# Kernel tuning notes

Hardware: AMD Instinct MI355X
Metric: run time of the kernel (lower is better)

## Reference

```python
import jax, jax.numpy as jnp
import numpy as np

B, S, H, DH = 2, 4096, 8, 64
D = H * DH


def setup_inputs() -> dict:
    key = jax.random.key(0)
    ks = jax.random.split(key, 6)
    std = 1.0 / np.sqrt(D)
    return {
        "x": jax.random.normal(ks[0], (B, S, D), dtype=jnp.float32),
        "Wq": jax.random.normal(ks[1], (D, D), dtype=jnp.float32) * std,
        "Wk": jax.random.normal(ks[2], (D, D), dtype=jnp.float32) * std,
        "Wv": jax.random.normal(ks[3], (D, D), dtype=jnp.float32) * std,
        "Wo": jax.random.normal(ks[4], (D, D), dtype=jnp.float32) * std,
        "bo": jnp.zeros((D,), dtype=jnp.float32),
    }


def reference(x, Wq, Wk, Wv, Wo, bo):
    scale = DH ** (-0.5)
    # torch Linear: y = x @ W.T
    q = x @ Wq.T  # [B,S,D]
    k = x @ Wk.T
    v = x @ Wv.T
    # split heads -> [B,H,S,Dh]
    q = q.reshape(B, S, H, DH).transpose(0, 2, 1, 3)
    k = k.reshape(B, S, H, DH).transpose(0, 2, 1, 3)
    v = v.reshape(B, S, H, DH).transpose(0, 2, 1, 3)
    score = jnp.einsum('bhqd,bhkd->bhqk', q, k) * scale  # [B,H,S,S]
    weights = jax.nn.softmax(score, axis=-1)
    attn = jnp.einsum('bhqk,bhkd->bhqd', weights, v)  # [B,H,S,Dh]
    h_ = attn.transpose(0, 2, 1, 3).reshape(B, S, D)
    return h_ @ Wo.T + bo
```

## Files before the change

### kernel.cpp

```cpp
#include <hip/hip_runtime.h>

#define LOG2E 1.44269504088896340736f

typedef unsigned short u16;
typedef __bf16 bf16x4_t __attribute__((ext_vector_type(4)));
typedef __bf16 bf16x8_t __attribute__((ext_vector_type(8)));
typedef float f32x4_t __attribute__((ext_vector_type(4)));

__device__ __forceinline__ f32x4_t mfma16(bf16x8_t a, bf16x8_t b, f32x4_t c) {
  return __builtin_amdgcn_mfma_f32_16x16x32_bf16(a, b, c, 0, 0, 0);
}

__device__ __forceinline__ void gl_lds16(const u16* g, u16* l) {
  __builtin_amdgcn_global_load_lds(
      (const __attribute__((address_space(1))) unsigned int*)g,
      (__attribute__((address_space(3))) unsigned int*)l, 16, 0, 0);
}

__global__ __launch_bounds__(256) void cast_kernel(
    const float* __restrict__ x, const float* __restrict__ Wq, const float* __restrict__ Wk,
    const float* __restrict__ Wv, const float* __restrict__ Wo,
    u16* __restrict__ Xb, u16* __restrict__ Wqb, u16* __restrict__ Wkb,
    u16* __restrict__ Wvb, u16* __restrict__ Wob) {
  const int bid = blockIdx.x;
  const float* src;
  u16* dst;
  float scale = 1.f;
  int rel;
  if (bid < 2048)      { src = x;  dst = Xb;  rel = bid; }
  else if (bid < 2176) { src = Wq; dst = Wqb; rel = bid - 2048; scale = 0.125f * LOG2E; }
  else if (bid < 2304) { src = Wk; dst = Wkb; rel = bid - 2176; }
  else if (bid < 2432) { src = Wv; dst = Wvb; rel = bid - 2304; }
  else                 { src = Wo; dst = Wob; rel = bid - 2432; }
  const int i = rel * 2048 + threadIdx.x * 8;
  f32x4_t a = *(const f32x4_t*)(src + i) * scale;
  f32x4_t b = *(const f32x4_t*)(src + i + 4) * scale;
  union { uint4 u; struct { bf16x4_t lo, hi; } s; } c;
  c.s.lo = __builtin_convertvector(a, bf16x4_t);
  c.s.hi = __builtin_convertvector(b, bf16x4_t);
  *(uint4*)(dst + i) = c.u;
}

template <int MODE>
__device__ __forceinline__ void gemm_core_bf16(const u16* __restrict__ A, const u16* __restrict__ Bt,
                                               void* __restrict__ Cout, const float* __restrict__ bo,
                                               int Mbase, int Nbase) {
  __shared__ __align__(16) u16 smem[128 * 128];
  u16 (*As)[64] = (u16(*)[64])smem;
  u16 (*Bs)[64] = (u16(*)[64])(smem + 128 * 64);
  const int t = threadIdx.x;
  const int wave = t >> 6, lane = t & 63;
  const int r = lane & 15, qd = lane >> 4;
  const int wm = wave & 1, wn = wave >> 1;
  const int rr = lane >> 3;
  const int s8 = ((lane & 7) ^ (rr & 7)) * 8;

  f32x4_t acc[4][4];
#pragma unroll
  for (int i = 0; i < 4; i++)
#pragma unroll
    for (int j = 0; j < 4; j++) { f32x4_t z = {0.f, 0.f, 0.f, 0.f}; acc[i][j] = z; }

  const u16* pa = A  + (Mbase + wave * 32 + rr) * 512 + s8;
  const u16* pb = Bt + (Nbase + wave * 32 + rr) * 512 + s8;
  u16* la = &As[wave * 32][0];
  u16* lb = &Bs[wave * 32][0];

  for (int k0 = 0; k0 < 512; k0 += 64) {
#pragma unroll
    for (int j = 0; j < 4; j++) gl_lds16(pa + k0 + j * 8 * 512, la + j * 8 * 64);
#pragma unroll
    for (int j = 0; j < 4; j++) gl_lds16(pb + k0 + j * 8 * 512, lb + j * 8 * 64);
    __syncthreads();
#pragma unroll
    for (int h = 0; h < 2; h++) {
      bf16x8_t af[4], bfr[4];
#pragma unroll
      for (int i = 0; i < 4; i++)
        af[i]  = *(const bf16x8_t*)&As[wm * 64 + i * 16 + r][((h * 4 + qd) ^ (r & 7)) * 8];
#pragma unroll
      for (int j = 0; j < 4; j++)
        bfr[j] = *(const bf16x8_t*)&Bs[wn * 64 + j * 16 + r][((h * 4 + qd) ^ (r & 7)) * 8];
#pragma unroll
      for (int i = 0; i < 4; i++)
#pragma unroll
        for (int j = 0; j < 4; j++) acc[i][j] = mfma16(af[i], bfr[j], acc[i][j]);
    }
    __syncthreads();
  }

  if (MODE != 2) {
#pragma unroll
    for (int i = 0; i < 4; i++)
#pragma unroll
      for (int j = 0; j < 4; j++)
#pragma unroll
        for (int reg = 0; reg < 4; reg++) {
          int row = wm * 64 + i * 16 + qd * 4 + reg;
          int col = wn * 64 + j * 16 + r;
          __bf16 bv = (__bf16)acc[i][j][reg];
          smem[row * 128 + (col ^ (((row >> 2) & 7) << 3))] = *(u16*)&bv;
        }
    __syncthreads();
#pragma unroll
    for (int p = 0; p < 8; p++) {
      int row = p * 16 + (t >> 4);
      int col = (t & 15) * 8;
      uint4 v = *(const uint4*)&smem[row * 128 + (col ^ (((row >> 2) & 7) << 3))];
      if (MODE == 0) {
        *(uint4*)&((u16*)Cout)[(Mbase + row) * 512 + Nbase + col] = v;
      } else {
        int bb = Nbase >> 12;
        int ss = (Nbase & 4095) + col;
        *(uint4*)&((u16*)Cout)[((long)(bb * 512 + Mbase + row)) * 4096 + ss] = v;
      }
    }
  } else {
    float* stf = (float*)smem;
    float bv[4];
#pragma unroll
    for (int j = 0; j < 4; j++) bv[j] = bo[Nbase + wn * 64 + j * 16 + r];
#pragma unroll
    for (int hh = 0; hh < 2; hh++) {
      __syncthreads();
      if (wm == hh) {
#pragma unroll
        for (int i = 0; i < 4; i++)
#pragma unroll
          for (int j = 0; j < 4; j++)
#pragma unroll
            for (int reg = 0; reg < 4; reg++) {
              int row = i * 16 + qd * 4 + reg;
              int col = wn * 64 + j * 16 + r;
              stf[row * 128 + (col ^ (((row >> 2) & 7) << 2))] = acc[i][j][reg] + bv[j];
            }
      }
      __syncthreads();
#pragma unroll
      for (int p = 0; p < 4; p++) {
        int row = p * 16 + (t >> 4);
        int col = (t & 15) * 8;
        f32x4_t v0 = *(const f32x4_t*)&stf[row * 128 + ((col) ^ (((row >> 2) & 7) << 2))];
        f32x4_t v1 = *(const f32x4_t*)&stf[row * 128 + ((col + 4) ^ (((row >> 2) & 7) << 2))];
        *(f32x4_t*)&((float*)Cout)[(Mbase + hh * 64 + row) * 512 + Nbase + col] = v0;
        *(f32x4_t*)&((float*)Cout)[(Mbase + hh * 64 + row) * 512 + Nbase + col + 4] = v1;
      }
    }
  }
}

__global__ __launch_bounds__(256) void gemm_qkv_kernel(
    const u16* __restrict__ Xb,
    const u16* __restrict__ Wqb, const u16* __restrict__ Wkb, const u16* __restrict__ Wvb,
    u16* __restrict__ Q, u16* __restrict__ K, u16* __restrict__ Vt) {
  if (blockIdx.z == 0)
    gemm_core_bf16<0>(Xb, Wqb, Q, nullptr, blockIdx.x * 128, blockIdx.y * 128);
  else if (blockIdx.z == 1)
    gemm_core_bf16<0>(Xb, Wkb, K, nullptr, blockIdx.x * 128, blockIdx.y * 128);
  else
    gemm_core_bf16<1>(Wvb, Xb, Vt, nullptr, blockIdx.y * 128, blockIdx.x * 128);
}

__global__ __launch_bounds__(256) void gemm_out_kernel(
    const u16* __restrict__ Aat, const u16* __restrict__ Wob,
    float* __restrict__ Out, const float* __restrict__ bo) {
  gemm_core_bf16<2>(Aat, Wob, Out, bo, blockIdx.x * 128, blockIdx.y * 128);
}

__global__ __launch_bounds__(512, 2) void attn_kernel(
    const u16* __restrict__ Q, const u16* __restrict__ K, const u16* __restrict__ Vt,
    u16* __restrict__ Oattn) {
  __shared__ __align__(16) u16 KVs[32768];
  __shared__ float Lsc2[1024];
#define KS(kvv, bf) (KVs + ((kvv) * 2 + (bf)) * 4096)
#define VS(kvv, bf) (KVs + 16384 + ((kvv) * 2 + (bf)) * 4096)

  const int t = threadIdx.x;
  const int wave = t >> 6, lane = t & 63;
  const int r = lane & 15, qd = lane >> 4;
  const int g = wave >> 1, kv = wave & 1;

  const int flat = blockIdx.y * 16 + blockIdx.x;
  const int xcd = flat & 7, idx = flat >> 3;
  const int bh = xcd * 2 + (idx >> 4);
  const int qi = idx & 15;
  const int b = bh >> 3, h = bh & 7;
  const long bbase = (long)b * 4096 * 512;
  const int q0 = qi * 256;

  const int sw = r & 7;
  const int ck0 = (qd ^ sw) * 8;
  const int ck1 = ((qd + 4) ^ sw) * 8;
  int vo0[2], vo1[2];
#pragma unroll
  for (int c = 0; c < 2; c++) {
    vo0[c] = ((c * 4 + (qd >> 1)) ^ sw) * 8 + 4 * (qd & 1);
    vo1[c] = ((c * 4 + 2 + (qd >> 1)) ^ sw) * 8 + 4 * (qd & 1);
  }

  bf16x8_t ones8;
#pragma unroll
  for (int j = 0; j < 8; j++) ones8[j] = (__bf16)1.0f;

  bf16x8_t qf[4][2];
#pragma unroll
  for (int qa = 0; qa < 4; qa++) {
    const u16* qp = Q + bbase + (long)(q0 + g * 64 + qa * 16 + r) * 512 + h * 64 + qd * 8;
    qf[qa][0] = *(const bf16x8_t*)(qp);
    qf[qa][1] = *(const bf16x8_t*)(qp + 32);
  }

  f32x4_t accO[4][4];
  f32x4_t accL[4];
#pragma unroll
  for (int qa = 0; qa < 4; qa++) {
    f32x4_t z = {0.f, 0.f, 0.f, 0.f};
    accL[qa] = z;
#pragma unroll
    for (int nt = 0; nt < 4; nt++) accO[qa][nt] = z;
  }

  const int rr = lane >> 3;
  const int cc = (lane & 7) ^ rr;
  const u16* kgb = K + bbase + (long)(kv * 2048 + g * 16 + rr) * 512 + h * 64 + cc * 8;
  const u16* vgb = Vt + ((long)(b * 512 + h * 64 + g * 16 + rr)) * 4096 + kv * 2048 + cc * 8;

#pragma unroll
  for (int i = 0; i < 2; i++) gl_lds16(kgb + (long)i * 8 * 512, KS(kv, 0) + g * 1024 + i * 512);
#pragma unroll
  for (int i = 0; i < 2; i++) gl_lds16(vgb + (long)i * 8 * 4096, VS(kv, 0) + g * 1024 + i * 512);

  for (int it = 0; it < 32; it++) {
    const int buf = it & 1;
    __syncthreads();

    if (it < 31) {
      const int nb = (it + 1) & 1;
      const long ko = (long)(it + 1) * 64;
#pragma unroll
      for (int i = 0; i < 2; i++)
        gl_lds16(kgb + (ko + i * 8) * 512, KS(kv, nb) + g * 1024 + i * 512);
#pragma unroll
      for (int i = 0; i < 2; i++)
        gl_lds16(vgb + ko + (long)i * 8 * 4096, VS(kv, nb) + g * 1024 + i * 512);
    }

    bf16x8_t kf[4][2];
#pragma unroll
    for (int nt = 0; nt < 4; nt++) {
      const u16* kb = KS(kv, buf) + (nt * 16 + r) * 64;
      kf[nt][0] = *(const bf16x8_t*)(kb + ck0);
      kf[nt][1] = *(const bf16x8_t*)(kb + ck1);
    }

    f32x4_t St[4][4];
    __builtin_amdgcn_s_setprio(1);
#pragma unroll
    for (int qa = 0; qa < 4; qa++)
#pragma unroll
      for (int nt = 0; nt < 4; nt++) {
        f32x4_t z = {0.f, 0.f, 0.f, 0.f};
        z = mfma16(kf[nt][0], qf[qa][0], z);
        z = mfma16(kf[nt][1], qf[qa][1], z);
        St[qa][nt] = z;
      }
    __builtin_amdgcn_s_setprio(0);

    bf16x8_t pf[4][2];
#pragma unroll
    for (int qa = 0; qa < 4; qa++)
#pragma unroll
      for (int c = 0; c < 2; c++) {
        f32x4_t e0, e1;
#pragma unroll
        for (int j = 0; j < 4; j++) {
          e0[j] = __builtin_amdgcn_exp2f(St[qa][2 * c][j]);
          e1[j] = __builtin_amdgcn_exp2f(St[qa][2 * c + 1][j]);
        }
        bf16x4_t b0 = __builtin_convertvector(e0, bf16x4_t);
        bf16x4_t b1 = __builtin_convertvector(e1, bf16x4_t);
        bf16x8_t p8;
#pragma unroll
        for (int j = 0; j < 4; j++) { p8[j] = b0[j]; p8[4 + j] = b1[j]; }
        pf[qa][c] = p8;
      }

#pragma unroll
    for (int qa = 0; qa < 4; qa++)
#pragma unroll
      for (int c = 0; c < 2; c++)
        accL[qa] = mfma16(ones8, pf[qa][c], accL[qa]);

#pragma unroll
    for (int c = 0; c < 2; c++) {
      bf16x8_t va[4];
#pragma unroll
      for (int dm = 0; dm < 4; dm++) {
        const u16* vb = VS(kv, buf) + (dm * 16 + r) * 64;
        union { uint4 u; bf16x8_t v; } cat;
        *(uint2*)&cat.u.x = *(const uint2*)(vb + vo0[c]);
        *(uint2*)&cat.u.z = *(const uint2*)(vb + vo1[c]);
        va[dm] = cat.v;
      }
      __builtin_amdgcn_s_setprio(1);
#pragma unroll
      for (int qa = 0; qa < 4; qa++)
#pragma unroll
        for (int dm = 0; dm < 4; dm++)
          accO[qa][dm] = mfma16(va[dm], pf[qa][c], accO[qa][dm]);
      __builtin_amdgcn_s_setprio(0);
    }
  }

  __syncthreads();
  float* Sc = (float*)KVs;
  if (kv == 1) {
#pragma unroll
    for (int qa = 0; qa < 4; qa++) {
#pragma unroll
      for (int dm = 0; dm < 4; dm++)
        *(f32x4_t*)&Sc[g * 4096 + ((qa * 4 + dm) * 64 + lane) * 4] = accO[qa][dm];
      Lsc2[g * 256 + qa * 64 + lane] = accL[qa][0];
    }
  }
  __syncthreads();
  if (kv == 0) {
#pragma unroll
    for (int qa = 0; qa < 4; qa++) {
      float L = accL[qa][0] + Lsc2[g * 256 + qa * 64 + lane];
      float inv = 1.f / L;
      int gq = q0 + g * 64 + qa * 16 + r;
#pragma unroll
      for (int dm = 0; dm < 4; dm++) {
        f32x4_t o = *(const f32x4_t*)&Sc[g * 4096 + ((qa * 4 + dm) * 64 + lane) * 4];
        o += accO[qa][dm];
        bf16x4_t ob;
#pragma unroll
        for (int reg = 0; reg < 4; reg++) ob[reg] = (__bf16)(o[reg] * inv);
        *(uint2*)&Oattn[bbase + (long)gq * 512 + h * 64 + dm * 16 + qd * 4] = *(uint2*)&ob;
      }
    }
  }
#undef KS
#undef VS
}

extern "C" void kernel_launch(void* const* d_in, const int* in_sizes, int n_in,
                              void* d_out, int out_size, void* d_ws, size_t ws_size,
                              hipStream_t stream) {
  const float* x  = (const float*)d_in[0];
  const float* Wq = (const float*)d_in[1];
  const float* Wk = (const float*)d_in[2];
  const float* Wv = (const float*)d_in[3];
  const float* Wo = (const float*)d_in[4];
  const float* bo = (const float*)d_in[5];
  float* out = (float*)d_out;

  u16* ws  = (u16*)d_ws;
  u16* Qb  = ws;
  u16* Kb  = Qb  + 4194304;
  u16* Vtg = Kb  + 4194304;
  u16* Ab  = Vtg + 4194304;
  u16* Xb  = Ab;
  u16* Wqb = Ab  + 4194304;
  u16* Wkb = Wqb + 262144;
  u16* Wvb = Wkb + 262144;
  u16* Wob = Wvb + 262144;

  cast_kernel<<<2560, 256, 0, stream>>>(x, Wq, Wk, Wv, Wo, Xb, Wqb, Wkb, Wvb, Wob);

  dim3 g1(64, 4, 3);
  gemm_qkv_kernel<<<g1, 256, 0, stream>>>(Xb, Wqb, Wkb, Wvb, Qb, Kb, Vtg);

  dim3 g2(16, 16);
  attn_kernel<<<g2, 512, 0, stream>>>(Qb, Kb, Vtg, Ab);

  dim3 g3(64, 4);
  gemm_out_kernel<<<g3, 256, 0, stream>>>(Ab, Wob, out, bo);
}
```

Before: 192.3 us.

## Software-pipeline QK^T one tile ahead with triple-buffered K in attention

Restructures the attention loop so the QK^T scores for the next KV tile are computed while the softmax exp and PV MFMAs of the current tile run. K is triple-buffered in LDS (prefetched two tiles ahead) and V stays double-buffered, which raises LDS use per block. The aim is to overlap exp/VALU work with matrix-core work and hide LDS latency. It costs extra registers for two score sets, which risks spills or lower occupancy under launch_bounds(512,2).

```diff
diff --git a/kernel.cpp b/kernel.cpp
--- a/kernel.cpp
+++ b/kernel.cpp
@@ -170,10 +170,8 @@
 __global__ __launch_bounds__(512, 2) void attn_kernel(
     const u16* __restrict__ Q, const u16* __restrict__ K, const u16* __restrict__ Vt,
     u16* __restrict__ Oattn) {
-  __shared__ __align__(16) u16 KVs[32768];
+  __shared__ __align__(16) u16 KVs[40960];
   __shared__ float Lsc2[1024];
-#define KS(kvv, bf) (KVs + ((kvv) * 2 + (bf)) * 4096)
-#define VS(kvv, bf) (KVs + 16384 + ((kvv) * 2 + (bf)) * 4096)
 
   const int t = threadIdx.x;
   const int wave = t >> 6, lane = t & 63;
@@ -191,11 +189,11 @@
   const int sw = r & 7;
   const int ck0 = (qd ^ sw) * 8;
   const int ck1 = ((qd + 4) ^ sw) * 8;
-  int vo0[2], vo1[2];
+  int vof0[2], vof1[2];
 #pragma unroll
   for (int c = 0; c < 2; c++) {
-    vo0[c] = ((c * 4 + (qd >> 1)) ^ sw) * 8 + 4 * (qd & 1);
-    vo1[c] = ((c * 4 + 2 + (qd >> 1)) ^ sw) * 8 + 4 * (qd & 1);
+    vof0[c] = ((c * 4 + (qd >> 1)) ^ sw) * 8 + 4 * (qd & 1);
+    vof1[c] = ((c * 4 + 2 + (qd >> 1)) ^ sw) * 8 + 4 * (qd & 1);
   }
 
   bf16x8_t ones8;
@@ -224,82 +222,98 @@
   const int cc = (lane & 7) ^ rr;
   const u16* kgb = K + bbase + (long)(kv * 2048 + g * 16 + rr) * 512 + h * 64 + cc * 8;
   const u16* vgb = Vt + ((long)(b * 512 + h * 64 + g * 16 + rr)) * 4096 + kv * 2048 + cc * 8;
-
-#pragma unroll
-  for (int i = 0; i < 2; i++) gl_lds16(kgb + (long)i * 8 * 512, KS(kv, 0) + g * 1024 + i * 512);
-#pragma unroll
-  for (int i = 0; i < 2; i++) gl_lds16(vgb + (long)i * 8 * 4096, VS(kv, 0) + g * 1024 + i * 512);
-
-  for (int it = 0; it < 32; it++) {
-    const int buf = it & 1;
-    __syncthreads();
-
+  u16* kst = KVs + kv * 4096 + g * 1024;
+  u16* vst = KVs + 24576 + kv * 4096 + g * 1024;
+  const u16* krd = KVs + kv * 4096;
+  const u16* vrd = KVs + 24576 + kv * 4096;
+
+#pragma unroll
+  for (int i = 0; i < 2; i++) gl_lds16(kgb + (long)i * 8 * 512, kst + i * 512);
+#pragma unroll
+  for (int i = 0; i < 2; i++) gl_lds16(kgb + (long)(64 + i * 8) * 512, kst + 8192 + i * 512);
+#pragma unroll
+  for (int i = 0; i < 2; i++) gl_lds16(vgb + (long)i * 8 * 4096, vst + i * 512);
+  __syncthreads();
+
+  f32x4_t Sa[4][4], Sb[4][4];
+
+  __builtin_amdgcn_s_setprio(1);
+#pragma unroll
+  for (int nt = 0; nt < 4; nt++) {
+    const u16* kb = krd + (nt * 16 + r) * 64;
+    bf16x8_t kf0 = *(const bf16x8_t*)(kb + ck0);
+    bf16x8_t kf1 = *(const bf16x8_t*)(kb + ck1);
+#pragma unroll
+    for (int qa = 0; qa < 4; qa++) {
+      f32x4_t z = {0.f, 0.f, 0.f, 0.f};
+      z = mfma16(kf0, qf[qa][0], z);
+      z = mfma16(kf1, qf[qa][1], z);
+      Sa[qa][nt] = z;
+    }
+  }
+  __builtin_amdgcn_s_setprio(0);
+
+  int kr = 1, kw = 2;
+
+  auto body = [&](int it, f32x4_t (&Sp)[4][4], f32x4_t (&Sn)[4][4]) {
+    if (it < 30) {
+      const long ko = (long)(it + 2) * 64;
+      u16* kd = kst + kw * 8192;
+#pragma unroll
+      for (int i = 0; i < 2; i++) gl_lds16(kgb + (ko + i * 8) * 512, kd + i * 512);
+    }
     if (it < 31) {
-      const int nb = (it + 1) & 1;
-      const long ko = (long)(it + 1) * 64;
-#pragma unroll
-      for (int i = 0; i < 2; i++)
-        gl_lds16(kgb + (ko + i * 8) * 512, KS(kv, nb) + g * 1024 + i * 512);
-#pragma unroll
-      for (int i = 0; i < 2; i++)
-        gl_lds16(vgb + ko + (long)i * 8 * 4096, VS(kv, nb) + g * 1024 + i * 512);
-    }
-
-    bf16x8_t kf[4][2];
-#pragma unroll
-    for (int nt = 0; nt < 4; nt++) {
-      const u16* kb = KS(kv, buf) + (nt * 16 + r) * 64;
-      kf[nt][0] = *(const bf16x8_t*)(kb + ck0);
-      kf[nt][1] = *(const bf16x8_t*)(kb + ck1);
-    }
-
-    f32x4_t St[4][4];
-    __builtin_amdgcn_s_setprio(1);
-#pragma unroll
-    for (int qa = 0; qa < 4; qa++)
+      const long vo = (long)(it + 1) * 64;
+      u16* vd = vst + ((it + 1) & 1) * 8192;
+#pragma unroll
+      for (int i = 0; i < 2; i++) gl_lds16(vgb + vo + (long)i * 8 * 4096, vd + i * 512);
+    }
+    if (it < 31) {
+      const u16* kbb = krd + kr * 8192;
+      __builtin_amdgcn_s_setprio(1);
 #pragma unroll
       for (int nt = 0; nt < 4; nt++) {
-        f32x4_t z = {0.f, 0.f, 0.f, 0.f};
-        z = mfma16(kf[nt][0], qf[qa][0], z);
-        z = mfma16(kf[nt][1], qf[qa][1], z);
-        St[qa][nt] = z;
-      }
-    __builtin_amdgcn_s_setprio(0);
-
-    bf16x8_t pf[4][2];
-#pragma unroll
-    for (int qa = 0; qa < 4; qa++)
-#pragma unroll
-      for (int c = 0; c < 2; c++) {
+        const u16* kb = kbb + (nt * 16 + r) * 64;
+        bf16x8_t kf0 = *(const bf16x8_t*)(kb + ck0);
+        bf16x8_t kf1 = *(const bf16x8_t*)(kb + ck1);
+#pragma unroll
+        for (int qa = 0; qa < 4; qa++) {
+          f32x4_t z = {0.f, 0.f, 0.f, 0.f};
+          z = mfma16(kf0, qf[qa][0], z);
+          z = mfma16(kf1, qf[qa][1], z);
+          Sn[qa][nt] = z;
+        }
+      }
+      __builtin_amdgcn_s_setprio(0);
+    }
+    const u16* vbb = vrd + (it & 1) * 8192;
+#pragma unroll
+    for (int c = 0; c < 2; c++) {
+      bf16x8_t pf[4];
+#pragma unroll
+      for (int qa = 0; qa < 4; qa++) {
         f32x4_t e0, e1;
 #pragma unroll
         for (int j = 0; j < 4; j++) {
-          e0[j] = __builtin_amdgcn_exp2f(St[qa][2 * c][j]);
-          e1[j] = __builtin_amdgcn_exp2f(St[qa][2 * c + 1][j]);
+          e0[j] = __builtin_amdgcn_exp2f(Sp[qa][2 * c][j]);
+          e1[j] = __builtin_amdgcn_exp2f(Sp[qa][2 * c + 1][j]);
         }
         bf16x4_t b0 = __builtin_convertvector(e0, bf16x4_t);
         bf16x4_t b1 = __builtin_convertvector(e1, bf16x4_t);
         bf16x8_t p8;
 #pragma unroll
         for (int j = 0; j < 4; j++) { p8[j] = b0[j]; p8[4 + j] = b1[j]; }
-        pf[qa][c] = p8;
-      }
-
-#pragma unroll
-    for (int qa = 0; qa < 4; qa++)
-#pragma unroll
-      for (int c = 0; c < 2; c++)
-        accL[qa] = mfma16(ones8, pf[qa][c], accL[qa]);
-
-#pragma unroll
-    for (int c = 0; c < 2; c++) {
+        pf[qa] = p8;
+      }
+#pragma unroll
+      for (int qa = 0; qa < 4; qa++) accL[qa] = mfma16(ones8, pf[qa], accL[qa]);
       bf16x8_t va[4];
 #pragma unroll
       for (int dm = 0; dm < 4; dm++) {
-        const u16* vb = VS(kv, buf) + (dm * 16 + r) * 64;
+        const u16* vb = vbb + (dm * 16 + r) * 64;
         union { uint4 u; bf16x8_t v; } cat;
-        *(uint2*)&cat.u.x = *(const uint2*)(vb + vo0[c]);
-        *(uint2*)&cat.u.z = *(const uint2*)(vb + vo1[c]);
+        *(uint2*)&cat.u.x = *(const uint2*)(vb + vof0[c]);
+        *(uint2*)&cat.u.z = *(const uint2*)(vb + vof1[c]);
         va[dm] = cat.v;
       }
       __builtin_amdgcn_s_setprio(1);
@@ -307,12 +321,19 @@
       for (int qa = 0; qa < 4; qa++)
 #pragma unroll
         for (int dm = 0; dm < 4; dm++)
-          accO[qa][dm] = mfma16(va[dm], pf[qa][c], accO[qa][dm]);
+          accO[qa][dm] = mfma16(va[dm], pf[qa], accO[qa][dm]);
       __builtin_amdgcn_s_setprio(0);
     }
-  }
-
-  __syncthreads();
+    __syncthreads();
+  };
+
+  for (int it2 = 0; it2 < 32; it2 += 2) {
+    body(it2, Sa, Sb);
+    { int nk = 3 - kr - kw; kr = kw; kw = nk; }
+    body(it2 + 1, Sb, Sa);
+    { int nk = 3 - kr - kw; kr = kw; kw = nk; }
+  }
+
   float* Sc = (float*)KVs;
   if (kv == 1) {
 #pragma unroll
@@ -341,8 +362,6 @@
       }
     }
   }
-#undef KS
-#undef VS
 }
 
 extern "C" void kernel_launch(void* const* d_in, const int* in_sizes, int n_in,
```

New measurement: 308.5 us. 60.4% more time.

## Shrink attention blocks to 64 queries with 4 waves for more parallelism

Applied to the files above, without the earlier changes.

Restructures the attention kernel from 512-thread blocks covering 256 queries to 256-thread blocks covering 64 queries. Each wave now handles 32 queries and a 32-key slice per 64-key step, and the K/V tile staging and swizzle are rearranged to match. The grid grows fourfold to 1024 blocks so more CUs are busy and occupancy goes up. In exchange each K/V tile is reused by fewer queries, so global and LDS traffic per unit of work rises and there are more barriers per unit of MFMA work.

```diff
diff --git a/kernel.cpp b/kernel.cpp
--- a/kernel.cpp
+++ b/kernel.cpp
@@ -167,98 +167,102 @@
   gemm_core_bf16<2>(Aat, Wob, Out, bo, blockIdx.x * 128, blockIdx.y * 128);
 }
 
-__global__ __launch_bounds__(512, 2) void attn_kernel(
+__global__ __launch_bounds__(256, 4) void attn_kernel(
     const u16* __restrict__ Q, const u16* __restrict__ K, const u16* __restrict__ Vt,
     u16* __restrict__ Oattn) {
-  __shared__ __align__(16) u16 KVs[32768];
-  __shared__ float Lsc2[1024];
-#define KS(kvv, bf) (KVs + ((kvv) * 2 + (bf)) * 4096)
-#define VS(kvv, bf) (KVs + 16384 + ((kvv) * 2 + (bf)) * 4096)
+  __shared__ __align__(16) u16 KVs[16384];
+  __shared__ float Lsc2[256];
 
   const int t = threadIdx.x;
   const int wave = t >> 6, lane = t & 63;
   const int r = lane & 15, qd = lane >> 4;
   const int g = wave >> 1, kv = wave & 1;
 
-  const int flat = blockIdx.y * 16 + blockIdx.x;
+  const int flat = blockIdx.y * 64 + blockIdx.x;
   const int xcd = flat & 7, idx = flat >> 3;
-  const int bh = xcd * 2 + (idx >> 4);
-  const int qi = idx & 15;
+  const int bh = xcd * 2 + (idx >> 6);
+  const int qi = idx & 63;
   const int b = bh >> 3, h = bh & 7;
   const long bbase = (long)b * 4096 * 512;
-  const int q0 = qi * 256;
+  const int q0 = qi * 64;
 
   const int sw = r & 7;
   const int ck0 = (qd ^ sw) * 8;
   const int ck1 = ((qd + 4) ^ sw) * 8;
   int vo0[2], vo1[2];
 #pragma unroll
-  for (int c = 0; c < 2; c++) {
-    vo0[c] = ((c * 4 + (qd >> 1)) ^ sw) * 8 + 4 * (qd & 1);
-    vo1[c] = ((c * 4 + 2 + (qd >> 1)) ^ sw) * 8 + 4 * (qd & 1);
+  for (int dh2 = 0; dh2 < 2; dh2++) {
+    vo0[dh2] = (((dh2 * 4 + (qd >> 1))) ^ sw) * 8 + (qd & 1) * 4;
+    vo1[dh2] = (((dh2 * 4 + 2 + (qd >> 1))) ^ sw) * 8 + (qd & 1) * 4;
   }
 
   bf16x8_t ones8;
 #pragma unroll
   for (int j = 0; j < 8; j++) ones8[j] = (__bf16)1.0f;
 
-  bf16x8_t qf[4][2];
-#pragma unroll
-  for (int qa = 0; qa < 4; qa++) {
-    const u16* qp = Q + bbase + (long)(q0 + g * 64 + qa * 16 + r) * 512 + h * 64 + qd * 8;
+  bf16x8_t qf[2][2];
+#pragma unroll
+  for (int qa = 0; qa < 2; qa++) {
+    const u16* qp = Q + bbase + (long)(q0 + g * 32 + qa * 16 + r) * 512 + h * 64 + qd * 8;
     qf[qa][0] = *(const bf16x8_t*)(qp);
     qf[qa][1] = *(const bf16x8_t*)(qp + 32);
   }
 
-  f32x4_t accO[4][4];
-  f32x4_t accL[4];
-#pragma unroll
-  for (int qa = 0; qa < 4; qa++) {
+  f32x4_t accO[2][4];
+  f32x4_t accL[2];
+#pragma unroll
+  for (int qa = 0; qa < 2; qa++) {
     f32x4_t z = {0.f, 0.f, 0.f, 0.f};
     accL[qa] = z;
 #pragma unroll
-    for (int nt = 0; nt < 4; nt++) accO[qa][nt] = z;
+    for (int dm = 0; dm < 4; dm++) accO[qa][dm] = z;
   }
 
   const int rr = lane >> 3;
-  const int cc = (lane & 7) ^ rr;
-  const u16* kgb = K + bbase + (long)(kv * 2048 + g * 16 + rr) * 512 + h * 64 + cc * 8;
-  const u16* vgb = Vt + ((long)(b * 512 + h * 64 + g * 16 + rr)) * 4096 + kv * 2048 + cc * 8;
-
-#pragma unroll
-  for (int i = 0; i < 2; i++) gl_lds16(kgb + (long)i * 8 * 512, KS(kv, 0) + g * 1024 + i * 512);
-#pragma unroll
-  for (int i = 0; i < 2; i++) gl_lds16(vgb + (long)i * 8 * 4096, VS(kv, 0) + g * 1024 + i * 512);
-
-  for (int it = 0; it < 32; it++) {
+  const int cc = lane & 7;
+  const int sg = cc ^ rr;
+  const u16* kgb = K + bbase + (long)(kv * 32 + g * 16 + rr) * 512 + h * 64 + sg * 8;
+  const u16* vgb = Vt + ((long)(b * 512 + h * 64 + (sg >> 2) * 32 + g * 16 + rr)) * 4096 +
+                   kv * 32 + (sg & 3) * 8;
+  u16* kst = KVs + kv * 4096 + g * 1024;
+  u16* vst = KVs + 8192 + kv * 4096 + g * 1024;
+  const u16* krd = KVs + kv * 4096;
+  const u16* vrd = KVs + 8192 + kv * 4096;
+
+#pragma unroll
+  for (int i = 0; i < 2; i++) gl_lds16(kgb + (long)i * 8 * 512, kst + i * 512);
+#pragma unroll
+  for (int i = 0; i < 2; i++) gl_lds16(vgb + (long)i * 8 * 4096, vst + i * 512);
+
+  for (int it = 0; it < 64; it++) {
     const int buf = it & 1;
     __syncthreads();
 
-    if (it < 31) {
+    if (it < 63) {
       const int nb = (it + 1) & 1;
       const long ko = (long)(it + 1) * 64;
 #pragma unroll
       for (int i = 0; i < 2; i++)
-        gl_lds16(kgb + (ko + i * 8) * 512, KS(kv, nb) + g * 1024 + i * 512);
+        gl_lds16(kgb + (ko + i * 8) * 512, kst + nb * 2048 + i * 512);
 #pragma unroll
       for (int i = 0; i < 2; i++)
-        gl_lds16(vgb + ko + (long)i * 8 * 4096, VS(kv, nb) + g * 1024 + i * 512);
-    }
-
-    bf16x8_t kf[4][2];
-#pragma unroll
-    for (int nt = 0; nt < 4; nt++) {
-      const u16* kb = KS(kv, buf) + (nt * 16 + r) * 64;
+        gl_lds16(vgb + ko + (long)i * 8 * 4096, vst + nb * 2048 + i * 512);
+    }
+
+    bf16x8_t kf[2][2];
+#pragma unroll
+    for (int nt = 0; nt < 2; nt++) {
+      const u16* kb = krd + buf * 2048 + (nt * 16 + r) * 64;
       kf[nt][0] = *(const bf16x8_t*)(kb + ck0);
       kf[nt][1] = *(const bf16x8_t*)(kb + ck1);
     }
 
-    f32x4_t St[4][4];
+    f32x4_t St[2][2];
     __builtin_amdgcn_s_setprio(1);
 #pragma unroll
-    for (int qa = 0; qa < 4; qa++)
-#pragma unroll
-      for (int nt = 0; nt < 4; nt++) {
+    for (int qa = 0; qa < 2; qa++)
+#pragma unroll
+      for (int nt = 0; nt < 2; nt++) {
         f32x4_t z = {0.f, 0.f, 0.f, 0.f};
         z = mfma16(kf[nt][0], qf[qa][0], z);
         z = mfma16(kf[nt][1], qf[qa][1], z);
@@ -266,73 +270,65 @@
       }
     __builtin_amdgcn_s_setprio(0);
 
-    bf16x8_t pf[4][2];
-#pragma unroll
-    for (int qa = 0; qa < 4; qa++)
-#pragma unroll
-      for (int c = 0; c < 2; c++) {
-        f32x4_t e0, e1;
-#pragma unroll
-        for (int j = 0; j < 4; j++) {
-          e0[j] = __builtin_amdgcn_exp2f(St[qa][2 * c][j]);
-          e1[j] = __builtin_amdgcn_exp2f(St[qa][2 * c + 1][j]);
-        }
-        bf16x4_t b0 = __builtin_convertvector(e0, bf16x4_t);
-        bf16x4_t b1 = __builtin_convertvector(e1, bf16x4_t);
-        bf16x8_t p8;
-#pragma unroll
-        for (int j = 0; j < 4; j++) { p8[j] = b0[j]; p8[4 + j] = b1[j]; }
-        pf[qa][c] = p8;
-      }
-
-#pragma unroll
-    for (int qa = 0; qa < 4; qa++)
-#pragma unroll
-      for (int c = 0; c < 2; c++)
-        accL[qa] = mfma16(ones8, pf[qa][c], accL[qa]);
-
-#pragma unroll
-    for (int c = 0; c < 2; c++) {
-      bf16x8_t va[4];
-#pragma unroll
-      for (int dm = 0; dm < 4; dm++) {
-        const u16* vb = VS(kv, buf) + (dm * 16 + r) * 64;
-        union { uint4 u; bf16x8_t v; } cat;
-        *(uint2*)&cat.u.x = *(const uint2*)(vb + vo0[c]);
-        *(uint2*)&cat.u.z = *(const uint2*)(vb + vo1[c]);
-        va[dm] = cat.v;
-      }
-      __builtin_amdgcn_s_setprio(1);
-#pragma unroll
-      for (int qa = 0; qa < 4; qa++)
-#pragma unroll
-        for (int dm = 0; dm < 4; dm++)
-          accO[qa][dm] = mfma16(va[dm], pf[qa][c], accO[qa][dm]);
-      __builtin_amdgcn_s_setprio(0);
-    }
+    bf16x8_t pf[2];
+#pragma unroll
+    for (int qa = 0; qa < 2; qa++) {
+      f32x4_t e0, e1;
+#pragma unroll
+      for (int j = 0; j < 4; j++) {
+        e0[j] = __builtin_amdgcn_exp2f(St[qa][0][j]);
+        e1[j] = __builtin_amdgcn_exp2f(St[qa][1][j]);
+      }
+      bf16x4_t b0 = __builtin_convertvector(e0, bf16x4_t);
+      bf16x4_t b1 = __builtin_convertvector(e1, bf16x4_t);
+      bf16x8_t p8;
+#pragma unroll
+      for (int j = 0; j < 4; j++) { p8[j] = b0[j]; p8[4 + j] = b1[j]; }
+      pf[qa] = p8;
+    }
+
+#pragma unroll
+    for (int qa = 0; qa < 2; qa++) accL[qa] = mfma16(ones8, pf[qa], accL[qa]);
+
+    bf16x8_t va[4];
+#pragma unroll
+    for (int dm = 0; dm < 4; dm++) {
+      const u16* vb = vrd + buf * 2048 + ((dm & 1) * 16 + r) * 64;
+      union { uint4 u; bf16x8_t v; } cat;
+      *(uint2*)&cat.u.x = *(const uint2*)(vb + vo0[dm >> 1]);
+      *(uint2*)&cat.u.z = *(const uint2*)(vb + vo1[dm >> 1]);
+      va[dm] = cat.v;
+    }
+    __builtin_amdgcn_s_setprio(1);
+#pragma unroll
+    for (int qa = 0; qa < 2; qa++)
+#pragma unroll
+      for (int dm = 0; dm < 4; dm++)
+        accO[qa][dm] = mfma16(va[dm], pf[qa], accO[qa][dm]);
+    __builtin_amdgcn_s_setprio(0);
   }
 
   __syncthreads();
   float* Sc = (float*)KVs;
   if (kv == 1) {
 #pragma unroll
-    for (int qa = 0; qa < 4; qa++) {
+    for (int qa = 0; qa < 2; qa++) {
 #pragma unroll
       for (int dm = 0; dm < 4; dm++)
-        *(f32x4_t*)&Sc[g * 4096 + ((qa * 4 + dm) * 64 + lane) * 4] = accO[qa][dm];
-      Lsc2[g * 256 + qa * 64 + lane] = accL[qa][0];
+        *(f32x4_t*)&Sc[g * 2048 + ((qa * 4 + dm) * 64 + lane) * 4] = accO[qa][dm];
+      Lsc2[g * 128 + qa * 64 + lane] = accL[qa][0];
     }
   }
   __syncthreads();
   if (kv == 0) {
 #pragma unroll
-    for (int qa = 0; qa < 4; qa++) {
-      float L = accL[qa][0] + Lsc2[g * 256 + qa * 64 + lane];
+    for (int qa = 0; qa < 2; qa++) {
+      float L = accL[qa][0] + Lsc2[g * 128 + qa * 64 + lane];
       float inv = 1.f / L;
-      int gq = q0 + g * 64 + qa * 16 + r;
+      int gq = q0 + g * 32 + qa * 16 + r;
 #pragma unroll
       for (int dm = 0; dm < 4; dm++) {
-        f32x4_t o = *(const f32x4_t*)&Sc[g * 4096 + ((qa * 4 + dm) * 64 + lane) * 4];
+        f32x4_t o = *(const f32x4_t*)&Sc[g * 2048 + ((qa * 4 + dm) * 64 + lane) * 4];
         o += accO[qa][dm];
         bf16x4_t ob;
 #pragma unroll
@@ -341,8 +337,6 @@
       }
     }
   }
-#undef KS
-#undef VS
 }
 
 extern "C" void kernel_launch(void* const* d_in, const int* in_sizes, int n_in,
@@ -372,8 +366,8 @@
   dim3 g1(64, 4, 3);
   gemm_qkv_kernel<<<g1, 256, 0, stream>>>(Xb, Wqb, Wkb, Wvb, Qb, Kb, Vtg);
 
-  dim3 g2(16, 16);
-  attn_kernel<<<g2, 512, 0, stream>>>(Qb, Kb, Vtg, Ab);
+  dim3 g2(64, 16);
+  attn_kernel<<<g2, 256, 0, stream>>>(Qb, Kb, Vtg, Ab);
 
   dim3 g3(64, 4);
   gemm_out_kernel<<<g3, 256, 0, stream>>>(Ab, Wob, out, bo);
```

New measurement: 199.5 us. 3.7% more time.
